# Optimization experiments

Measured on AMD Instinct MI355X. Metric: run time of the kernel, lower is better.

## Reference

```python
import jax, jax.numpy as jnp
import numpy as np
import math

DIM = 256
N = 4096
E = 1024
NEG = -1.0e9


def setup_inputs() -> dict:
    key = jax.random.key(0)
    ks = jax.random.split(key, 10)
    x = jax.random.normal(ks[0], (N, DIM), dtype=jnp.float32)
    # sparse incidence / adjacency (module only uses >0 as mask)
    H = (jax.random.uniform(ks[1], (N, E)) < 0.05).astype(jnp.float32)
    adj = (jax.random.uniform(ks[2], (N, N)) < 0.01).astype(jnp.float32)
    s = 1.0 / math.sqrt(DIM)
    W_he = jax.random.normal(ks[3], (DIM, DIM), dtype=jnp.float32) * s  # HyperedgeAttention.W
    u = jax.random.normal(ks[4], (DIM,), dtype=jnp.float32)            # HyperedgeAttention.u
    W_e = jax.random.normal(ks[5], (DIM, DIM), dtype=jnp.float32) * s  # NodeAttention.W_e
    W_n = jax.random.normal(ks[6], (DIM, DIM), dtype=jnp.float32) * s  # NodeAttention.W_n
    W_g = jax.random.normal(ks[7], (DIM, DIM), dtype=jnp.float32) * s  # GraphAttention.W
    a_g = jax.random.normal(ks[8], (2 * DIM,), dtype=jnp.float32) * s  # GraphAttention.attn weight
    return {"x": x, "H": H, "adj": adj, "W_he": W_he, "u": u,
            "W_e": W_e, "W_n": W_n, "W_g": W_g, "a_g": a_g}


def reference(x, H, adj, W_he, u, W_e, W_n, W_g, a_g):
    n, dim = x.shape
    inv_sqrt_d = 1.0 / math.sqrt(dim)
    maskH = H > 0                       # [N,E] bool
    mask_Hf = maskH.astype(x.dtype)

    # ---- HyperedgeAttention ----
    h_he = x @ W_he                     # [N,dim]
    sc = (h_he @ u) * inv_sqrt_d        # [N]
    scE = jnp.where(maskH, sc[:, None], NEG)      # [N,E]
    A = jax.nn.softmax(scE, axis=0) * mask_Hf     # column softmax over nodes
    e_repr = A.T @ h_he                 # [E,dim]

    # ---- NodeAttention (only B is used) ----
    hn = x @ W_n                        # [N,dim]
    he = e_repr @ W_e                   # [E,dim]
    Bsc = jnp.where(maskH, (hn @ he.T) * inv_sqrt_d, NEG)
    B = jax.nn.softmax(Bsc, axis=1) * mask_Hf     # [N,E]

    # ---- GraphAttention (concat score split: e_ij = lrelu(h_i.a1 + h_j.a2)) ----
    h_g = x @ W_g                       # [N,dim]
    s1 = h_g @ a_g[:dim]                # [N]
    s2 = h_g @ a_g[dim:]                # [N]
    e = jax.nn.leaky_relu(s1[:, None] + s2[None, :], 0.2)   # [N,N]
    maskA = (adj > 0).astype(x.dtype)
    sl = jnp.eye(n, dtype=x.dtype)
    e = e * (maskA + sl) - 1e9 * jnp.clip(1.0 - maskA - sl, 0.0, None)
    G = jax.nn.softmax(e, axis=1)       # [N,N]

    # ---- Mixing ----
    he_sz = jnp.clip(mask_Hf.sum(0), 1.0, None)   # [E]
    M = (G @ mask_Hf) / he_sz[None, :]            # [N,E]
    A_hat = jax.nn.softmax(A.T + M.T, axis=1) * mask_Hf.T   # [E,N]
    e_mix = A_hat @ (x @ W_he)                    # [E,dim]
    B_hat = jax.nn.softmax(B + M, axis=1) * mask_Hf          # [N,E]
    z_h = jax.nn.elu(B_hat @ (e_mix @ W_e))       # [N,dim]
    G_hat = jax.nn.softmax(G + B @ B.T + A @ A.T, axis=1)    # [N,N]
    z_g = jax.nn.elu(G_hat @ (x @ W_g))           # [N,dim]
    return z_h, z_g
```

## Files before the change

### kernel.cpp

```cpp
#include <hip/hip_runtime.h>
#include <math.h>
#include <stdint.h>

#define Nn 4096
#define Ee 1024
#define Dd 256

typedef __attribute__((ext_vector_type(8))) __bf16 bf16x8;
typedef __attribute__((ext_vector_type(4))) float f32x4;
typedef __attribute__((ext_vector_type(8))) unsigned short u16x8;

__device__ __forceinline__ unsigned short f2bf(float f) {
  unsigned int u = __float_as_uint(f);
  unsigned int r = (u + 0x7fffu + ((u >> 16) & 1u)) >> 16;
  return (unsigned short)r;
}
__device__ __forceinline__ float bf2f(unsigned short u) {
  return __uint_as_float(((unsigned int)u) << 16);
}

__device__ __forceinline__ void gload_lds16(const void* g, void* l) {
  __builtin_amdgcn_global_load_lds(
      (__attribute__((address_space(1))) void*)const_cast<void*>(g),
      (__attribute__((address_space(3))) void*)l, 16, 0, 0);
}

__device__ __forceinline__ float block_reduce_sum(float v) {
  __shared__ float sh[4];
  #pragma unroll
  for (int o = 32; o > 0; o >>= 1) v += __shfl_down(v, o);
  int lane = threadIdx.x & 63, w = threadIdx.x >> 6;
  if (lane == 0) sh[w] = v;
  __syncthreads();
  float s = sh[0] + sh[1] + sh[2] + sh[3];
  __syncthreads();
  return s;
}

__global__ __launch_bounds__(256) void gemm_bt_bf16(
    const unsigned short* __restrict__ Ab, const unsigned short* __restrict__ Bb,
    float* __restrict__ Cp, unsigned short* __restrict__ Cb,
    int M, int N, int K, int lda, int ldb, float alpha,
    const float* __restrict__ coldiv)
{
  __shared__ unsigned short As[2][128 * 32];
  __shared__ unsigned short Bs[2][128 * 32];
  const int tid = threadIdx.x;
  const int m0 = blockIdx.x * 128, n0 = blockIdx.y * 128;
  const int wave = tid >> 6, lane = tid & 63;
  const int wr = (wave >> 1) * 64, wc = (wave & 1) * 64;
  const int l16 = lane & 15, lq = lane >> 4;
  f32x4 acc[4][4] = {};
  const int NT = K >> 5;

  auto stage = [&](int buf, int kt) {
    const int k0 = kt * 32;
    #pragma unroll
    for (int i = 0; i < 2; ++i) {
      int t2 = tid + i * 256;
      int r = t2 >> 2, c = (t2 & 3) * 8;
      gload_lds16(Ab + (size_t)(m0 + r) * lda + k0 + c, &As[buf][t2 * 8]);
    }
    #pragma unroll
    for (int i = 0; i < 2; ++i) {
      int t2 = tid + i * 256;
      int r = t2 >> 2, c = (t2 & 3) * 8;
      gload_lds16(Bb + (size_t)(n0 + r) * ldb + k0 + c, &Bs[buf][t2 * 8]);
    }
  };

  stage(0, 0);
  __syncthreads();
  int buf = 0;
  for (int kt = 0; kt < NT; ++kt) {
    if (kt + 1 < NT) stage(buf ^ 1, kt + 1);
    bf16x8 af[4], bfr[4];
    #pragma unroll
    for (int m = 0; m < 4; ++m)
      af[m] = *reinterpret_cast<const bf16x8*>(&As[buf][(wr + m * 16 + l16) * 32 + lq * 8]);
    #pragma unroll
    for (int n = 0; n < 4; ++n)
      bfr[n] = *reinterpret_cast<const bf16x8*>(&Bs[buf][(wc + n * 16 + l16) * 32 + lq * 8]);
    #pragma unroll
    for (int m = 0; m < 4; ++m)
      #pragma unroll
      for (int n = 0; n < 4; ++n)
        acc[m][n] = __builtin_amdgcn_mfma_f32_16x16x32_bf16(af[m], bfr[n], acc[m][n], 0, 0, 0);
    __syncthreads();
    buf ^= 1;
  }
  #pragma unroll
  for (int m = 0; m < 4; ++m)
    #pragma unroll
    for (int n = 0; n < 4; ++n) {
      int col = n0 + wc + n * 16 + l16;
      float cd = coldiv ? fmaxf(coldiv[col], 1.f) : 1.f;
      #pragma unroll
      for (int q = 0; q < 4; ++q) {
        int row = m0 + wr + m * 16 + lq * 4 + q;
        size_t idx = (size_t)row * N + col;
        float v = acc[m][n][q] * alpha / cd;
        Cp[idx] = v;
        if (Cb) Cb[idx] = f2bf(v);
      }
    }
}

__global__ __launch_bounds__(256) void gemm_gram_k(
    const unsigned short* __restrict__ CAT,
    const float* __restrict__ G,
    unsigned short* __restrict__ Gb,
    float* __restrict__ rowsum)
{
  const int bx = blockIdx.x, by = blockIdx.y;
  if (bx > by) return;
  const int K = 2048;
  __shared__ unsigned short SM[17024];
  unsigned short* Asb = SM;
  unsigned short* Bsb = SM + 8192;
  const int tid = threadIdx.x;
  const int m0 = bx * 128, n0 = by * 128;
  const int wave = tid >> 6, lane = tid & 63;
  const int wr = (wave >> 1) * 64, wc = (wave & 1) * 64;
  const int l16 = lane & 15, lq = lane >> 4;
  f32x4 acc[4][4] = {};
  const int NT = K >> 5;

  auto stage = [&](int buf, int kt) {
    const int k0 = kt * 32;
    #pragma unroll
    for (int i = 0; i < 2; ++i) {
      int t2 = tid + i * 256;
      int r = t2 >> 2, c = (t2 & 3) * 8;
      gload_lds16(CAT + (size_t)(m0 + r) * K + k0 + c, Asb + buf * 4096 + t2 * 8);
    }
    #pragma unroll
    for (int i = 0; i < 2; ++i) {
      int t2 = tid + i * 256;
      int r = t2 >> 2, c = (t2 & 3) * 8;
      gload_lds16(CAT + (size_t)(n0 + r) * K + k0 + c, Bsb + buf * 4096 + t2 * 8);
    }
  };

  stage(0, 0);
  __syncthreads();
  int buf = 0;
  for (int kt = 0; kt < NT; ++kt) {
    if (kt + 1 < NT) stage(buf ^ 1, kt + 1);
    bf16x8 af[4], bfr[4];
    #pragma unroll
    for (int m = 0; m < 4; ++m)
      af[m] = *reinterpret_cast<const bf16x8*>(Asb + buf * 4096 + (wr + m * 16 + l16) * 32 + lq * 8);
    #pragma unroll
    for (int n = 0; n < 4; ++n)
      bfr[n] = *reinterpret_cast<const bf16x8*>(Bsb + buf * 4096 + (wc + n * 16 + l16) * 32 + lq * 8);
    #pragma unroll
    for (int m = 0; m < 4; ++m)
      #pragma unroll
      for (int n = 0; n < 4; ++n)
        acc[m][n] = __builtin_amdgcn_mfma_f32_16x16x32_bf16(af[m], bfr[n], acc[m][n], 0, 0, 0);
    __syncthreads();
    buf ^= 1;
  }
  #pragma unroll
  for (int m = 0; m < 4; ++m)
    #pragma unroll
    for (int q = 0; q < 4; ++q) {
      int row = m0 + wr + m * 16 + lq * 4 + q;
      float s = 0.f;
      #pragma unroll
      for (int n = 0; n < 4; ++n) {
        int col = n0 + wc + n * 16 + l16;
        size_t idx = (size_t)row * Nn + col;
        float e = expf(G[idx] + acc[m][n][q]);
        Gb[idx] = f2bf(e);
        s += e;
      }
      s += __shfl_xor(s, 1); s += __shfl_xor(s, 2);
      s += __shfl_xor(s, 4); s += __shfl_xor(s, 8);
      if (l16 == 0) atomicAdd(&rowsum[row], s);
    }
  if (bx == by) return;

  __syncthreads();
  unsigned short* Tg = SM;
  {
    int cc = tid >> 1, r0 = (tid & 1) * 64;
    const unsigned short* src = Gb + (size_t)(n0 + cc) * Nn + m0 + r0;
    unsigned short* dst = Tg + cc * 132 + r0;
    #pragma unroll
    for (int v = 0; v < 8; ++v)
      *reinterpret_cast<u16x8*>(dst + v * 8) = *reinterpret_cast<const u16x8*>(src + v * 8);
  }
  __syncthreads();
  #pragma unroll
  for (int n = 0; n < 4; ++n) {
    int ccl = wc + n * 16 + l16;
    float cs = 0.f;
    #pragma unroll
    for (int m = 0; m < 4; ++m) {
      int sa = ccl * 132 + wr + m * 16 + lq * 4;
      ushort4 lg = *reinterpret_cast<const ushort4*>(&Tg[sa]);
      ushort4 eo;
      float e0 = expf(bf2f(lg.x) + acc[m][n][0]); eo.x = f2bf(e0); cs += e0;
      float e1 = expf(bf2f(lg.y) + acc[m][n][1]); eo.y = f2bf(e1); cs += e1;
      float e2 = expf(bf2f(lg.z) + acc[m][n][2]); eo.z = f2bf(e2); cs += e2;
      float e3 = expf(bf2f(lg.w) + acc[m][n][3]); eo.w = f2bf(e3); cs += e3;
      *reinterpret_cast<ushort4*>(&Tg[sa]) = eo;
    }
    cs += __shfl_xor(cs, 16); cs += __shfl_xor(cs, 32);
    if (lq == 0) atomicAdd(&rowsum[n0 + ccl], cs);
  }
  __syncthreads();
  {
    int cc = tid >> 1, r0 = (tid & 1) * 64;
    const unsigned short* src = Tg + cc * 132 + r0;
    unsigned short* dst = Gb + (size_t)(n0 + cc) * Nn + m0 + r0;
    #pragma unroll
    for (int v = 0; v < 8; ++v)
      *reinterpret_cast<u16x8*>(dst + v * 8) = *reinterpret_cast<const u16x8*>(src + v * 8);
  }
}

__global__ __launch_bounds__(256) void gemm64s_bt_bf16(
    const unsigned short* __restrict__ Ab, const unsigned short* __restrict__ Bb,
    float* __restrict__ Cp, int M, int N, int K, int KS)
{
  __shared__ unsigned short As[2][64 * 64];
  __shared__ unsigned short Bs[2][64 * 64];
  const int tid = threadIdx.x;
  const int m0 = blockIdx.x * 64, n0 = blockIdx.y * 64;
  const int kbase = blockIdx.z * KS;
  const int wave = tid >> 6, lane = tid & 63;
  const int wr = (wave >> 1) * 32, wc = (wave & 1) * 32;
  const int l16 = lane & 15, lq = lane >> 4;
  f32x4 acc[2][2] = {};
  const int NT = KS >> 6;

  auto stage = [&](int buf, int kt) {
    const int k0 = kbase + kt * 64;
    #pragma unroll
    for (int i = 0; i < 2; ++i) {
      int t2 = tid + i * 256;
      int r = t2 >> 3, c = (t2 & 7) * 8;
      gload_lds16(Ab + (size_t)(m0 + r) * K + k0 + c, &As[buf][t2 * 8]);
    }
    #pragma unroll
    for (int i = 0; i < 2; ++i) {
      int t2 = tid + i * 256;
      int r = t2 >> 3, c = (t2 & 7) * 8;
      gload_lds16(Bb + (size_t)(n0 + r) * K + k0 + c, &Bs[buf][t2 * 8]);
    }
  };

  stage(0, 0);
  __syncthreads();
  int buf = 0;
  for (int kt = 0; kt < NT; ++kt) {
    if (kt + 1 < NT) stage(buf ^ 1, kt + 1);
    bf16x8 af[2][2], bfr[2][2];
    #pragma unroll
    for (int m = 0; m < 2; ++m)
      #pragma unroll
      for (int ks = 0; ks < 2; ++ks)
        af[m][ks] = *reinterpret_cast<const bf16x8*>(
            &As[buf][(wr + m * 16 + l16) * 64 + ks * 32 + lq * 8]);
    #pragma unroll
    for (int n = 0; n < 2; ++n)
      #pragma unroll
      for (int ks = 0; ks < 2; ++ks)
        bfr[n][ks] = *reinterpret_cast<const bf16x8*>(
            &Bs[buf][(wc + n * 16 + l16) * 64 + ks * 32 + lq * 8]);
    #pragma unroll
    for (int m = 0; m < 2; ++m)
      #pragma unroll
      for (int n = 0; n < 2; ++n)
        #pragma unroll
        for (int ks = 0; ks < 2; ++ks)
          acc[m][n] = __builtin_amdgcn_mfma_f32_16x16x32_bf16(af[m][ks], bfr[n][ks], acc[m][n], 0, 0, 0);
    __syncthreads();
    buf ^= 1;
  }
  #pragma unroll
  for (int m = 0; m < 2; ++m)
    #pragma unroll
    for (int n = 0; n < 2; ++n) {
      int col = n0 + wc + n * 16 + l16;
      #pragma unroll
      for (int q = 0; q < 4; ++q) {
        int row = m0 + wr + m * 16 + lq * 4 + q;
        atomicAdd(&Cp[(size_t)row * N + col], acc[m][n][q]);
      }
    }
}

__global__ __launch_bounds__(256) void cvt_bf16_k(const float* __restrict__ in,
                                                  unsigned short* __restrict__ out, long n) {
  long i = ((long)blockIdx.x * 256 + threadIdx.x) * 8;
  if (i + 8 > n) return;
  float4 a = *reinterpret_cast<const float4*>(&in[i]);
  float4 b = *reinterpret_cast<const float4*>(&in[i + 4]);
  u16x8 o;
  o[0] = f2bf(a.x); o[1] = f2bf(a.y); o[2] = f2bf(a.z); o[3] = f2bf(a.w);
  o[4] = f2bf(b.x); o[5] = f2bf(b.y); o[6] = f2bf(b.z); o[7] = f2bf(b.w);
  *reinterpret_cast<u16x8*>(&out[i]) = o;
}

__global__ __launch_bounds__(256) void tcvt_k(const float* __restrict__ in,
                                              unsigned short* __restrict__ outT, int R, int S) {
  __shared__ unsigned short tile[64][65];
  int r0 = blockIdx.x * 64, c0 = blockIdx.y * 64;
  int t = threadIdx.x & 63, q = threadIdx.x >> 6;
  for (int rr = q; rr < 64; rr += 4)
    tile[t][rr] = f2bf(in[(long)(r0 + rr) * S + c0 + t]);
  __syncthreads();
  for (int cc = q; cc < 64; cc += 4)
    outT[(long)(c0 + cc) * R + r0 + t] = tile[cc][t];
}

__global__ __launch_bounds__(256) void elu_rows_k(float* __restrict__ p,
                                                  const float* __restrict__ rowsum) {
  long i = ((long)blockIdx.x * 256 + threadIdx.x) * 4;
  float4 v = *reinterpret_cast<const float4*>(&p[i]);
  float sc = 1.f;
  long half = (long)Nn * Dd;
  if (i >= half) sc = 1.f / rowsum[(i - half) >> 8];
  v.x *= sc; v.y *= sc; v.z *= sc; v.w *= sc;
  v.x = v.x > 0.f ? v.x : expm1f(v.x);
  v.y = v.y > 0.f ? v.y : expm1f(v.y);
  v.z = v.z > 0.f ? v.z : expm1f(v.z);
  v.w = v.w > 0.f ? v.w : expm1f(v.w);
  *reinterpret_cast<float4*>(&p[i]) = v;
}

__global__ __launch_bounds__(256) void gemm64_k(
    const float* __restrict__ Ap, const float* __restrict__ Bp, float* __restrict__ Cp,
    unsigned short* __restrict__ Cb,
    int M, int N, int K, int Asm, int Ask, int Bsk, int Bsn)
{
  __shared__ alignas(16) float As[16][68];
  __shared__ alignas(16) float Bs[16][68];
  const int tid = threadIdx.x;
  const int tx = tid & 15, ty = tid >> 4;
  const int m0 = blockIdx.x * 64, n0 = blockIdx.y * 64;
  float acc[4][4] = {};
  for (int k0 = 0; k0 < K; k0 += 16) {
    if (Ask == 1) {
      int mm = tid >> 2, kk = (tid & 3) << 2;
      float4 v = *reinterpret_cast<const float4*>(&Ap[(long)(m0 + mm) * Asm + k0 + kk]);
      As[kk + 0][mm] = v.x; As[kk + 1][mm] = v.y; As[kk + 2][mm] = v.z; As[kk + 3][mm] = v.w;
    } else {
      int kk = tid >> 4, mm = (tid & 15) << 2;
      *reinterpret_cast<float4*>(&As[kk][mm]) =
          *reinterpret_cast<const float4*>(&Ap[(long)(k0 + kk) * Ask + m0 + mm]);
    }
    if (Bsn == 1) {
      int kk = tid >> 4, nn = (tid & 15) << 2;
      *reinterpret_cast<float4*>(&Bs[kk][nn]) =
          *reinterpret_cast<const float4*>(&Bp[(long)(k0 + kk) * Bsk + n0 + nn]);
    } else {
      int nn = tid >> 2, kk = (tid & 3) << 2;
      float4 v = *reinterpret_cast<const float4*>(&Bp[(long)(n0 + nn) * Bsn + k0 + kk]);
      Bs[kk + 0][nn] = v.x; Bs[kk + 1][nn] = v.y; Bs[kk + 2][nn] = v.z; Bs[kk + 3][nn] = v.w;
    }
    __syncthreads();
    #pragma unroll
    for (int kk = 0; kk < 16; ++kk) {
      float4 av = *reinterpret_cast<const float4*>(&As[kk][ty << 2]);
      float4 bv = *reinterpret_cast<const float4*>(&Bs[kk][tx << 2]);
      float a[4] = {av.x, av.y, av.z, av.w};
      float b[4] = {bv.x, bv.y, bv.z, bv.w};
      #pragma unroll
      for (int r = 0; r < 4; ++r)
        #pragma unroll
        for (int c = 0; c < 4; ++c) acc[r][c] = fmaf(a[r], b[c], acc[r][c]);
    }
    __syncthreads();
  }
  #pragma unroll
  for (int r = 0; r < 4; ++r) {
    long base = (long)(m0 + (ty << 2) + r) * N + n0 + (tx << 2);
    float4 o = {acc[r][0], acc[r][1], acc[r][2], acc[r][3]};
    *reinterpret_cast<float4*>(&Cp[base]) = o;
    if (Cb) {
      ushort4 ob = {f2bf(o.x), f2bf(o.y), f2bf(o.z), f2bf(o.w)};
      *reinterpret_cast<ushort4*>(&Cb[base]) = ob;
    }
  }
}

__global__ __launch_bounds__(256) void rowdots_k(
    const float* __restrict__ hcat, const float* __restrict__ u, const float* __restrict__ a_g,
    float* __restrict__ esc, float* __restrict__ s1, float* __restrict__ s2)
{
  int i = blockIdx.x, t = threadIdx.x;
  float hh = hcat[(long)i * 768 + t];
  float hg = hcat[(long)i * 768 + 512 + t];
  float d0 = block_reduce_sum(hh * u[t]);
  float d1 = block_reduce_sum(hg * a_g[t]);
  float d2 = block_reduce_sum(hg * a_g[Dd + t]);
  if (t == 0) {
    esc[i] = expf(d0 * 0.0625f);
    s1[i] = d1;
    s2[i] = d2;
  }
}

__global__ __launch_bounds__(256) void colstats_k(
    const float* __restrict__ H, const float* __restrict__ esc,
    float* __restrict__ colden, float* __restrict__ cnt)
{
  int e = blockIdx.x * 256 + threadIdx.x;
  int r0 = blockIdx.y * 128;
  float d = 0.f, c = 0.f;
  for (int r = r0; r < r0 + 128; ++r) {
    float h = H[(long)r * Ee + e];
    if (h > 0.f) { d += esc[r]; c += 1.f; }
  }
  atomicAdd(&colden[e], d);
  atomicAdd(&cnt[e], c);
}

__global__ __launch_bounds__(256) void fillA_k(
    const float* __restrict__ H, const float* __restrict__ esc,
    const float* __restrict__ colden, float* __restrict__ A,
    unsigned short* __restrict__ CAT, unsigned short* __restrict__ AbT)
{
  __shared__ unsigned short tile[64][68];
  int r0 = blockIdx.x * 64, e0 = blockIdx.y * 64;
  int te = threadIdx.x & 63, tq = threadIdx.x >> 6;
  float cd = colden[e0 + te];
  for (int rr = tq; rr < 64; rr += 4) {
    long idx = (long)(r0 + rr) * Ee + e0 + te;
    float h = H[idx];
    float val = h > 0.f ? esc[r0 + rr] / cd : 0.f;
    A[idx] = val;
    unsigned short vb = f2bf(val);
    CAT[(long)(r0 + rr) * 2048 + 1024 + e0 + te] = vb;
    tile[te][rr] = vb;
  }
  __syncthreads();
  for (int ee = tq; ee < 64; ee += 4)
    AbT[(long)(e0 + ee) * Nn + r0 + te] = tile[ee][te];
}

__global__ __launch_bounds__(256) void brow_k(float* __restrict__ Bbuf,
                                              const float* __restrict__ H,
                                              unsigned short* __restrict__ CAT)
{
  int i = blockIdx.x, t = threadIdx.x;
  long base = (long)i * Ee + t * 4;
  float4 raw = *reinterpret_cast<const float4*>(&Bbuf[base]);
  float4 h = *reinterpret_cast<const float4*>(&H[base]);
  float rr[4] = {raw.x, raw.y, raw.z, raw.w}, hh[4] = {h.x, h.y, h.z, h.w};
  float p[4]; float s = 0.f;
  #pragma unroll
  for (int k = 0; k < 4; ++k) { p[k] = hh[k] > 0.f ? expf(rr[k]) : 0.f; s += p[k]; }
  float den = block_reduce_sum(s);
  float inv = den > 0.f ? 1.f / den : 0.f;
  float4 o = {p[0] * inv, p[1] * inv, p[2] * inv, p[3] * inv};
  *reinterpret_cast<float4*>(&Bbuf[base]) = o;
  ushort4 ob = {f2bf(o.x), f2bf(o.y), f2bf(o.z), f2bf(o.w)};
  *reinterpret_cast<ushort4*>(&CAT[(long)i * 2048 + t * 4]) = ob;
}

__global__ __launch_bounds__(256) void gfill_k(
    const float* __restrict__ adj, const float* __restrict__ s1,
    const float* __restrict__ s2, float* __restrict__ G, unsigned short* __restrict__ Gb)
{
  int i = blockIdx.x, t = threadIdx.x;
  float s1i = s1[i];
  float p[16]; float sum = 0.f;
  #pragma unroll
  for (int c = 0; c < 4; ++c) {
    int j = c * 1024 + t * 4;
    float4 a = *reinterpret_cast<const float4*>(&adj[(long)i * Nn + j]);
    float4 sv = *reinterpret_cast<const float4*>(&s2[j]);
    float aa[4] = {a.x, a.y, a.z, a.w}, ss[4] = {sv.x, sv.y, sv.z, sv.w};
    #pragma unroll
    for (int k = 0; k < 4; ++k) {
      float f = (aa[k] > 0.f ? 1.f : 0.f) + ((j + k) == i ? 1.f : 0.f);
      float l = s1i + ss[k];
      l = l > 0.f ? l : 0.2f * l;
      float val = l * f - 1e9f * fmaxf(1.f - f, 0.f);
      float pp = expf(val);
      p[c * 4 + k] = pp; sum += pp;
    }
  }
  float den = block_reduce_sum(sum);
  float inv = 1.f / den;
  #pragma unroll
  for (int c = 0; c < 4; ++c) {
    int j = c * 1024 + t * 4;
    float4 o = {p[c * 4] * inv, p[c * 4 + 1] * inv, p[c * 4 + 2] * inv, p[c * 4 + 3] * inv};
    *reinterpret_cast<float4*>(&G[(long)i * Nn + j]) = o;
    ushort4 ob = {f2bf(o.x), f2bf(o.y), f2bf(o.z), f2bf(o.w)};
    *reinterpret_cast<ushort4*>(&Gb[(long)i * Nn + j]) = ob;
  }
}

__global__ __launch_bounds__(256) void amstats_k(
    const float* __restrict__ A, const float* __restrict__ Mm, float* __restrict__ aden)
{
  int e = blockIdx.x * 256 + threadIdx.x;
  int r0 = blockIdx.y * 128;
  float d = 0.f;
  for (int r = r0; r < r0 + 128; ++r) {
    long idx = (long)r * Ee + e;
    d += expf(A[idx] + Mm[idx]);
  }
  atomicAdd(&aden[e], d);
}

__global__ __launch_bounds__(256) void ahat_k(
    const float* __restrict__ Abuf, const float* __restrict__ Mm,
    const float* __restrict__ H, const float* __restrict__ aden,
    unsigned short* __restrict__ AhB)
{
  __shared__ float tile[64][65];
  int j0 = blockIdx.x * 64, e0 = blockIdx.y * 64;
  int te = threadIdx.x & 63;
  int tq = threadIdx.x >> 6;
  int e = e0 + te;
  float inv = 1.f / aden[e];
  for (int jj = tq; jj < 64; jj += 4) {
    long idx = (long)(j0 + jj) * Ee + e;
    float val = (H[idx] > 0.f) ? expf(Abuf[idx] + Mm[idx]) * inv : 0.f;
    tile[te][jj] = val;
  }
  __syncthreads();
  for (int ee = tq; ee < 64; ee += 4)
    AhB[(long)(e0 + ee) * Nn + j0 + te] = f2bf(tile[ee][te]);
}

__global__ __launch_bounds__(256) void bhat_k(const float* __restrict__ Bbuf,
                                              const float* __restrict__ Mm,
                                              const float* __restrict__ H,
                                              unsigned short* __restrict__ Bb2)
{
  int i = blockIdx.x, t = threadIdx.x;
  long base = (long)i * Ee + t * 4;
  float4 b = *reinterpret_cast<const float4*>(&Bbuf[base]);
  float4 m = *reinterpret_cast<const float4*>(&Mm[base]);
  float4 h = *reinterpret_cast<const float4*>(&H[base]);
  float bb[4] = {b.x, b.y, b.z, b.w}, mm2[4] = {m.x, m.y, m.z, m.w}, hh[4] = {h.x, h.y, h.z, h.w};
  float p[4]; float s = 0.f;
  #pragma unroll
  for (int k = 0; k < 4; ++k) { p[k] = expf(bb[k] + mm2[k]); s += p[k]; }
  float den = block_reduce_sum(s);
  float inv = 1.f / den;
  #pragma unroll
  for (int k = 0; k < 4; ++k) p[k] = hh[k] > 0.f ? p[k] * inv : 0.f;
  ushort4 ob = {f2bf(p[0]), f2bf(p[1]), f2bf(p[2]), f2bf(p[3])};
  *reinterpret_cast<ushort4*>(&Bb2[base]) = ob;
}

extern "C" void kernel_launch(void* const* d_in, const int* in_sizes, int n_in,
                              void* d_out, int out_size, void* d_ws, size_t ws_size,
                              hipStream_t stream) {
  const float* x    = (const float*)d_in[0];
  const float* H    = (const float*)d_in[1];
  const float* adj  = (const float*)d_in[2];
  const float* W_he = (const float*)d_in[3];
  const float* u    = (const float*)d_in[4];
  const float* W_e  = (const float*)d_in[5];
  const float* W_n  = (const float*)d_in[6];
  const float* W_g  = (const float*)d_in[7];
  const float* a_g  = (const float*)d_in[8];
  float* out = (float*)d_out;
  float* ws  = (float*)d_ws;
  (void)in_sizes; (void)n_in; (void)out_size; (void)ws_size;

  size_t off = 0;
  auto alloc = [&](size_t n) { float* p = ws + off; off += n; return p; };
  float* hcat   = alloc((size_t)Nn * 768);
  float* esc    = alloc(Nn);
  float* s1     = alloc(Nn);
  float* s2     = alloc(Nn);
  float* colden = alloc(Ee);
  float* cnt    = alloc(Ee);
  float* aden   = alloc(Ee);
  float* rowsum = alloc(Nn);
  float* e_repr = alloc((size_t)Ee * Dd);
  float* e_mix  = alloc((size_t)Ee * Dd);
  float* heb    = alloc((size_t)Ee * Dd);
  float* tmp_ew = alloc((size_t)Ee * Dd);
  float* Abuf   = alloc((size_t)Nn * Ee);
  float* Bbuf   = alloc((size_t)Nn * Ee);
  float* Mm     = alloc((size_t)Nn * Ee);
  float* G      = alloc((size_t)Nn * Nn);
  unsigned short* Gb    = (unsigned short*)alloc((size_t)Nn * Nn / 2);
  unsigned short* CAT   = (unsigned short*)alloc((size_t)Nn * 2048 / 2);
  unsigned short* Hbt   = (unsigned short*)alloc((size_t)Ee * Nn / 2);
  unsigned short* AbT   = (unsigned short*)alloc((size_t)Ee * Nn / 2);
  unsigned short* AhB   = (unsigned short*)alloc((size_t)Ee * Nn / 2);
  unsigned short* hheT  = (unsigned short*)alloc((size_t)Dd * Nn / 2);
  unsigned short* hgT   = (unsigned short*)alloc((size_t)Dd * Nn / 2);
  unsigned short* tewT  = (unsigned short*)alloc((size_t)Dd * Ee / 2);
  unsigned short* Bb2   = (unsigned short*)alloc((size_t)Nn * Ee / 2);
  unsigned short* xb    = (unsigned short*)alloc((size_t)Nn * Dd / 2);
  unsigned short* WcTb  = (unsigned short*)alloc((size_t)768 * Dd / 2);
  unsigned short* hcatB = (unsigned short*)alloc((size_t)Nn * 768 / 2);
  unsigned short* hebB  = (unsigned short*)alloc((size_t)Ee * Dd / 2);

  hipMemsetAsync(colden, 0, (3 * Ee + Nn) * sizeof(float), stream);
  hipMemsetAsync(e_repr, 0, 2 * (size_t)Ee * Dd * sizeof(float), stream);
  hipMemsetAsync(out, 0, 2 * (size_t)Nn * Dd * sizeof(float), stream);

  auto gbt = [&](const unsigned short* A, const unsigned short* B, float* C, unsigned short* Cb,
                 int M, int N, int K, int lda, int ldb, float alpha, const float* cd) {
    gemm_bt_bf16<<<dim3(M / 128, N / 128), 256, 0, stream>>>(A, B, C, Cb, M, N, K, lda, ldb,
                                                             alpha, cd);
  };
  auto gs64 = [&](const unsigned short* A, const unsigned short* B, float* C,
                  int M, int N, int K, int KS) {
    gemm64s_bt_bf16<<<dim3(M / 64, N / 64, K / KS), 256, 0, stream>>>(A, B, C, M, N, K, KS);
  };
  auto tcvt = [&](const float* in, unsigned short* o, int R, int S, int cols) {
    tcvt_k<<<dim3(R / 64, cols / 64), 256, 0, stream>>>(in, o, R, S);
  };

  cvt_bf16_k<<<(Nn * Dd) / 2048, 256, 0, stream>>>(x, xb, (long)Nn * Dd);
  tcvt(W_he, WcTb, Dd, Dd, Dd);
  tcvt(W_n, WcTb + 256 * 256, Dd, Dd, Dd);
  tcvt(W_g, WcTb + 2 * 256 * 256, Dd, Dd, Dd);
  gbt(xb, WcTb, hcat, hcatB, Nn, 768, Dd, Dd, Dd, 1.f, nullptr);
  rowdots_k<<<Nn, 256, 0, stream>>>(hcat, u, a_g, esc, s1, s2);
  colstats_k<<<dim3(Ee / 256, 32), 256, 0, stream>>>(H, esc, colden, cnt);
  fillA_k<<<dim3(Nn / 64, Ee / 64), 256, 0, stream>>>(H, esc, colden, Abuf, CAT, AbT);
  tcvt(hcat, hheT, Nn, 768, Dd);
  gs64(AbT, hheT, e_repr, Ee, Dd, Nn, 1024);
  gemm64_k<<<dim3(Ee / 64, Dd / 64), 256, 0, stream>>>(e_repr, W_e, heb, hebB, Ee, Dd, Dd, Dd, 1, Dd, 1);
  gbt(hcatB + 256, hebB, Bbuf, nullptr, Nn, Ee, Dd, 768, Dd, 0.0625f, nullptr);
  brow_k<<<Nn, 256, 0, stream>>>(Bbuf, H, CAT);
  gfill_k<<<Nn, 256, 0, stream>>>(adj, s1, s2, G, Gb);
  tcvt(H, Hbt, Nn, Ee, Ee);
  gbt(Gb, Hbt, Mm, nullptr, Nn, Ee, Nn, Nn, Nn, 1.f, cnt);
  gemm_gram_k<<<dim3(Nn / 128, Nn / 128), 256, 0, stream>>>(CAT, G, Gb, rowsum);
  amstats_k<<<dim3(Ee / 256, 32), 256, 0, stream>>>(Abuf, Mm, aden);
  ahat_k<<<dim3(Nn / 64, Ee / 64), 256, 0, stream>>>(Abuf, Mm, H, aden, AhB);
  gs64(AhB, hheT, e_mix, Ee, Dd, Nn, 1024);
  gemm64_k<<<dim3(Ee / 64, Dd / 64), 256, 0, stream>>>(e_mix, W_e, tmp_ew, nullptr, Ee, Dd, Dd, Dd, 1, Dd, 1);
  bhat_k<<<Nn, 256, 0, stream>>>(Bbuf, Mm, H, Bb2);
  tcvt(tmp_ew, tewT, Ee, Dd, Dd);
  gs64(Bb2, tewT, out, Nn, Dd, Ee, 1024);
  tcvt(hcat + 512, hgT, Nn, 768, Dd);
  gs64(Gb, hgT, out + (size_t)Nn * Dd, Nn, Dd, Nn, 2048);
  elu_rows_k<<<(2 * Nn * Dd) / 1024, 256, 0, stream>>>(out, rowsum);
}
```

Before: 665.4 us.

## Drop fp32 G buffer, split-K the M GEMM, fold column divide into transpose

Removes the fp32 N×N G matrix. gfill writes only the bf16 copy, and the gram kernel reads its G term back from bf16, which removes a large write and read of global memory. The G@H GEMM becomes a split-K kernel with atomic accumulation into a zeroed Mm buffer, and the per-column hyperedge-size division moves into the H transpose-convert. Split-K depth for several skinny GEMMs is halved to raise parallelism. In exchange the G values used in the gram softmax lose precision to bf16, and the new path adds atomics and a memset.

Result: faster. 618.2 us (-7.1%).

```diff
diff --git a/kernel.cpp b/kernel.cpp
--- a/kernel.cpp
+++ b/kernel.cpp
@@ -40,8 +40,7 @@
 __global__ __launch_bounds__(256) void gemm_bt_bf16(
     const unsigned short* __restrict__ Ab, const unsigned short* __restrict__ Bb,
     float* __restrict__ Cp, unsigned short* __restrict__ Cb,
-    int M, int N, int K, int lda, int ldb, float alpha,
-    const float* __restrict__ coldiv)
+    int M, int N, int K, int lda, int ldb, float alpha)
 {
   __shared__ unsigned short As[2][128 * 32];
   __shared__ unsigned short Bs[2][128 * 32];
@@ -94,21 +93,83 @@
     #pragma unroll
     for (int n = 0; n < 4; ++n) {
       int col = n0 + wc + n * 16 + l16;
-      float cd = coldiv ? fmaxf(coldiv[col], 1.f) : 1.f;
       #pragma unroll
       for (int q = 0; q < 4; ++q) {
         int row = m0 + wr + m * 16 + lq * 4 + q;
         size_t idx = (size_t)row * N + col;
-        float v = acc[m][n][q] * alpha / cd;
+        float v = acc[m][n][q] * alpha;
         Cp[idx] = v;
         if (Cb) Cb[idx] = f2bf(v);
       }
     }
 }
 
+__global__ __launch_bounds__(256) void gemm_bts_bf16(
+    const unsigned short* __restrict__ Ab, const unsigned short* __restrict__ Bb,
+    float* __restrict__ Cp, int M, int N, int K, int lda, int ldb, int KS)
+{
+  __shared__ unsigned short As[2][128 * 32];
+  __shared__ unsigned short Bs[2][128 * 32];
+  const int tid = threadIdx.x;
+  const int m0 = blockIdx.x * 128, n0 = blockIdx.y * 128;
+  const int kbase = blockIdx.z * KS;
+  const int wave = tid >> 6, lane = tid & 63;
+  const int wr = (wave >> 1) * 64, wc = (wave & 1) * 64;
+  const int l16 = lane & 15, lq = lane >> 4;
+  f32x4 acc[4][4] = {};
+  const int NT = KS >> 5;
+
+  auto stage = [&](int buf, int kt) {
+    const int k0 = kbase + kt * 32;
+    #pragma unroll
+    for (int i = 0; i < 2; ++i) {
+      int t2 = tid + i * 256;
+      int r = t2 >> 2, c = (t2 & 3) * 8;
+      gload_lds16(Ab + (size_t)(m0 + r) * lda + k0 + c, &As[buf][t2 * 8]);
+    }
+    #pragma unroll
+    for (int i = 0; i < 2; ++i) {
+      int t2 = tid + i * 256;
+      int r = t2 >> 2, c = (t2 & 3) * 8;
+      gload_lds16(Bb + (size_t)(n0 + r) * ldb + k0 + c, &Bs[buf][t2 * 8]);
+    }
+  };
+
+  stage(0, 0);
+  __syncthreads();
+  int buf = 0;
+  for (int kt = 0; kt < NT; ++kt) {
+    if (kt + 1 < NT) stage(buf ^ 1, kt + 1);
+    bf16x8 af[4], bfr[4];
+    #pragma unroll
+    for (int m = 0; m < 4; ++m)
+      af[m] = *reinterpret_cast<const bf16x8*>(&As[buf][(wr + m * 16 + l16) * 32 + lq * 8]);
+    #pragma unroll
+    for (int n = 0; n < 4; ++n)
+      bfr[n] = *reinterpret_cast<const bf16x8*>(&Bs[buf][(wc + n * 16 + l16) * 32 + lq * 8]);
+    #pragma unroll
+    for (int m = 0; m < 4; ++m)
+      #pragma unroll
+      for (int n = 0; n < 4; ++n)
+        acc[m][n] = __builtin_amdgcn_mfma_f32_16x16x32_bf16(af[m], bfr[n], acc[m][n], 0, 0, 0);
+    __syncthreads();
+    buf ^= 1;
+  }
+  #pragma unroll
+  for (int m = 0; m < 4; ++m)
+    #pragma unroll
+    for (int n = 0; n < 4; ++n) {
+      int col = n0 + wc + n * 16 + l16;
+      #pragma unroll
+      for (int q = 0; q < 4; ++q) {
+        int row = m0 + wr + m * 16 + lq * 4 + q;
+        atomicAdd(&Cp[(size_t)row * N + col], acc[m][n][q]);
+      }
+    }
+}
+
 __global__ __launch_bounds__(256) void gemm_gram_k(
     const unsigned short* __restrict__ CAT,
-    const float* __restrict__ G,
     unsigned short* __restrict__ Gb,
     float* __restrict__ rowsum)
 {
@@ -172,7 +233,7 @@
       for (int n = 0; n < 4; ++n) {
         int col = n0 + wc + n * 16 + l16;
         size_t idx = (size_t)row * Nn + col;
-        float e = expf(G[idx] + acc[m][n][q]);
+        float e = expf(bf2f(Gb[idx]) + acc[m][n][q]);
         Gb[idx] = f2bf(e);
         s += e;
       }
@@ -307,12 +368,14 @@
 }
 
 __global__ __launch_bounds__(256) void tcvt_k(const float* __restrict__ in,
-                                              unsigned short* __restrict__ outT, int R, int S) {
+                                              unsigned short* __restrict__ outT, int R, int S,
+                                              const float* __restrict__ coldiv) {
   __shared__ unsigned short tile[64][65];
   int r0 = blockIdx.x * 64, c0 = blockIdx.y * 64;
   int t = threadIdx.x & 63, q = threadIdx.x >> 6;
+  float sc = coldiv ? 1.f / fmaxf(coldiv[c0 + t], 1.f) : 1.f;
   for (int rr = q; rr < 64; rr += 4)
-    tile[t][rr] = f2bf(in[(long)(r0 + rr) * S + c0 + t]);
+    tile[t][rr] = f2bf(in[(long)(r0 + rr) * S + c0 + t] * sc);
   __syncthreads();
   for (int cc = q; cc < 64; cc += 4)
     outT[(long)(c0 + cc) * R + r0 + t] = tile[cc][t];
@@ -466,7 +529,7 @@
 
 __global__ __launch_bounds__(256) void gfill_k(
     const float* __restrict__ adj, const float* __restrict__ s1,
-    const float* __restrict__ s2, float* __restrict__ G, unsigned short* __restrict__ Gb)
+    const float* __restrict__ s2, unsigned short* __restrict__ Gb)
 {
   int i = blockIdx.x, t = threadIdx.x;
   float s1i = s1[i];
@@ -492,9 +555,8 @@
   #pragma unroll
   for (int c = 0; c < 4; ++c) {
     int j = c * 1024 + t * 4;
-    float4 o = {p[c * 4] * inv, p[c * 4 + 1] * inv, p[c * 4 + 2] * inv, p[c * 4 + 3] * inv};
-    *reinterpret_cast<float4*>(&G[(long)i * Nn + j]) = o;
-    ushort4 ob = {f2bf(o.x), f2bf(o.y), f2bf(o.z), f2bf(o.w)};
+    ushort4 ob = {f2bf(p[c * 4] * inv), f2bf(p[c * 4 + 1] * inv),
+                  f2bf(p[c * 4 + 2] * inv), f2bf(p[c * 4 + 3] * inv)};
     *reinterpret_cast<ushort4*>(&Gb[(long)i * Nn + j]) = ob;
   }
 }
@@ -588,7 +650,6 @@
   float* Abuf   = alloc((size_t)Nn * Ee);
   float* Bbuf   = alloc((size_t)Nn * Ee);
   float* Mm     = alloc((size_t)Nn * Ee);
-  float* G      = alloc((size_t)Nn * Nn);
   unsigned short* Gb    = (unsigned short*)alloc((size_t)Nn * Nn / 2);
   unsigned short* CAT   = (unsigned short*)alloc((size_t)Nn * 2048 / 2);
   unsigned short* Hbt   = (unsigned short*)alloc((size_t)Ee * Nn / 2);
@@ -605,46 +666,46 @@
 
   hipMemsetAsync(colden, 0, (3 * Ee + Nn) * sizeof(float), stream);
   hipMemsetAsync(e_repr, 0, 2 * (size_t)Ee * Dd * sizeof(float), stream);
+  hipMemsetAsync(Mm, 0, (size_t)Nn * Ee * sizeof(float), stream);
   hipMemsetAsync(out, 0, 2 * (size_t)Nn * Dd * sizeof(float), stream);
 
   auto gbt = [&](const unsigned short* A, const unsigned short* B, float* C, unsigned short* Cb,
-                 int M, int N, int K, int lda, int ldb, float alpha, const float* cd) {
-    gemm_bt_bf16<<<dim3(M / 128, N / 128), 256, 0, stream>>>(A, B, C, Cb, M, N, K, lda, ldb,
-                                                             alpha, cd);
+                 int M, int N, int K, int lda, int ldb, float alpha) {
+    gemm_bt_bf16<<<dim3(M / 128, N / 128), 256, 0, stream>>>(A, B, C, Cb, M, N, K, lda, ldb, alpha);
   };
   auto gs64 = [&](const unsigned short* A, const unsigned short* B, float* C,
                   int M, int N, int K, int KS) {
     gemm64s_bt_bf16<<<dim3(M / 64, N / 64, K / KS), 256, 0, stream>>>(A, B, C, M, N, K, KS);
   };
-  auto tcvt = [&](const float* in, unsigned short* o, int R, int S, int cols) {
-    tcvt_k<<<dim3(R / 64, cols / 64), 256, 0, stream>>>(in, o, R, S);
+  auto tcvt = [&](const float* in, unsigned short* o, int R, int S, int cols, const float* cd) {
+    tcvt_k<<<dim3(R / 64, cols / 64), 256, 0, stream>>>(in, o, R, S, cd);
   };
 
   cvt_bf16_k<<<(Nn * Dd) / 2048, 256, 0, stream>>>(x, xb, (long)Nn * Dd);
-  tcvt(W_he, WcTb, Dd, Dd, Dd);
-  tcvt(W_n, WcTb + 256 * 256, Dd, Dd, Dd);
-  tcvt(W_g, WcTb + 2 * 256 * 256, Dd, Dd, Dd);
-  gbt(xb, WcTb, hcat, hcatB, Nn, 768, Dd, Dd, Dd, 1.f, nullptr);
+  tcvt(W_he, WcTb, Dd, Dd, Dd, nullptr);
+  tcvt(W_n, WcTb + 256 * 256, Dd, Dd, Dd, nullptr);
+  tcvt(W_g, WcTb + 2 * 256 * 256, Dd, Dd, Dd, nullptr);
+  gbt(xb, WcTb, hcat, hcatB, Nn, 768, Dd, Dd, Dd, 1.f);
   rowdots_k<<<Nn, 256, 0, stream>>>(hcat, u, a_g, esc, s1, s2);
   colstats_k<<<dim3(Ee / 256, 32), 256, 0, stream>>>(H, esc, colden, cnt);
   fillA_k<<<dim3(Nn / 64, Ee / 64), 256, 0, stream>>>(H, esc, colden, Abuf, CAT, AbT);
-  tcvt(hcat, hheT, Nn, 768, Dd);
-  gs64(AbT, hheT, e_repr, Ee, Dd, Nn, 1024);
+  tcvt(hcat, hheT, Nn, 768, Dd, nullptr);
+  gs64(AbT, hheT, e_repr, Ee, Dd, Nn, 512);
   gemm64_k<<<dim3(Ee / 64, Dd / 64), 256, 0, stream>>>(e_repr, W_e, heb, hebB, Ee, Dd, Dd, Dd, 1, Dd, 1);
-  gbt(hcatB + 256, hebB, Bbuf, nullptr, Nn, Ee, Dd, 768, Dd, 0.0625f, nullptr);
+  gbt(hcatB + 256, hebB, Bbuf, nullptr, Nn, Ee, Dd, 768, Dd, 0.0625f);
   brow_k<<<Nn, 256, 0, stream>>>(Bbuf, H, CAT);
-  gfill_k<<<Nn, 256, 0, stream>>>(adj, s1, s2, G, Gb);
-  tcvt(H, Hbt, Nn, Ee, Ee);
-  gbt(Gb, Hbt, Mm, nullptr, Nn, Ee, Nn, Nn, Nn, 1.f, cnt);
-  gemm_gram_k<<<dim3(Nn / 128, Nn / 128), 256, 0, stream>>>(CAT, G, Gb, rowsum);
+  gfill_k<<<Nn, 256, 0, stream>>>(adj, s1, s2, Gb);
+  tcvt(H, Hbt, Nn, Ee, Ee, cnt);
+  gemm_bts_bf16<<<dim3(Nn / 128, Ee / 128, 2), 256, 0, stream>>>(Gb, Hbt, Mm, Nn, Ee, Nn, Nn, Nn, 2048);
+  gemm_gram_k<<<dim3(Nn / 128, Nn / 128), 256, 0, stream>>>(CAT, Gb, rowsum);
   amstats_k<<<dim3(Ee / 256, 32), 256, 0, stream>>>(Abuf, Mm, aden);
   ahat_k<<<dim3(Nn / 64, Ee / 64), 256, 0, stream>>>(Abuf, Mm, H, aden, AhB);
-  gs64(AhB, hheT, e_mix, Ee, Dd, Nn, 1024);
+  gs64(AhB, hheT, e_mix, Ee, Dd, Nn, 512);
   gemm64_k<<<dim3(Ee / 64, Dd / 64), 256, 0, stream>>>(e_mix, W_e, tmp_ew, nullptr, Ee, Dd, Dd, Dd, 1, Dd, 1);
   bhat_k<<<Nn, 256, 0, stream>>>(Bbuf, Mm, H, Bb2);
-  tcvt(tmp_ew, tewT, Ee, Dd, Dd);
-  gs64(Bb2, tewT, out, Nn, Dd, Ee, 1024);
-  tcvt(hcat + 512, hgT, Nn, 768, Dd);
-  gs64(Gb, hgT, out + (size_t)Nn * Dd, Nn, Dd, Nn, 2048);
+  tcvt(tmp_ew, tewT, Ee, Dd, Dd, nullptr);
+  gs64(Bb2, tewT, out, Nn, Dd, Ee, 512);
+  tcvt(hcat + 512, hgT, Nn, 768, Dd, nullptr);
+  gs64(Gb, hgT, out + (size_t)Nn * Dd, Nn, Dd, Nn, 1024);
   elu_rows_k<<<(2 * Nn * Dd) / 1024, 256, 0, stream>>>(out, rowsum);
 }
```
